# Kernel optimization log

Hardware: AMD Instinct MI355X
Metric: run time of the kernel (lower is better)

## Reference

```python
import jax, jax.numpy as jnp
import numpy as np
from math import lgamma

B = 8
RES = 64
RES_OUT = 32
L_IN = RES // 2 - 1        # 31
L_OUT = RES_OUT // 2 - 1   # 15
SPINS_IN = (0, 1)
SPINS_OUT = (0, 1, 2)
C_IN = 64
C_OUT = 128
K_IN = (L_IN + 1) ** 2     # 1024 coefficients, ordered by (ell, m): idx = ell^2 + (m + ell)
K_OUT = (L_OUT + 1) ** 2   # 256
EPS_BN = 1e-5
EPS_NL = 1e-6


def _wigner_d_col(l, s, thetas):
    """Wigner small-d column d^l_{m,-s}(theta) for m in [-l, l]; (2l+1, n_theta)."""
    n = -s
    out = np.zeros((2 * l + 1, thetas.size))
    if l < abs(s):
        return out
    cb = np.cos(thetas / 2.0)
    sb = np.sin(thetas / 2.0)
    for mi, m in enumerate(range(-l, l + 1)):
        pref = 0.5 * (lgamma(l + m + 1) + lgamma(l - m + 1)
                      + lgamma(l + n + 1) + lgamma(l - n + 1))
        acc = np.zeros_like(thetas)
        for k in range(max(0, n - m), min(l + n, l - m) + 1):
            lg = pref - (lgamma(l + n - k + 1) + lgamma(k + 1)
                         + lgamma(m - n + k + 1) + lgamma(l - m - k + 1))
            acc += ((-1.0) ** (m - n + k)) * np.exp(lg) \
                   * cb ** (2 * l + n - m - 2 * k) * sb ** (m - n + 2 * k)
        out[mi] = acc
    return out


def _sylm_grid(spin, ell_max, res):
    """Spin-weighted spherical harmonics sampled on equiangular grid: (K, res, res)."""
    thetas = (np.arange(res) + 0.5) * np.pi / res
    phis = np.arange(res) * 2.0 * np.pi / res
    Y = np.zeros(((ell_max + 1) ** 2, res, res), dtype=np.complex64)
    phase = np.exp(1j * np.outer(np.arange(-ell_max, ell_max + 1), phis))
    for l in range(ell_max + 1):
        d = _wigner_d_col(l, spin, thetas)               # (2l+1, res)
        norm = np.sqrt((2 * l + 1) / (4.0 * np.pi))
        for mi, m in enumerate(range(-l, l + 1)):
            Y[l * l + mi] = (((-1.0) ** m) * norm * d[mi][:, None]
                             * phase[m + ell_max][None, :])
    return Y


# Deterministic transform constants (computed once at import).
_THETA = (np.arange(RES) + 0.5) * np.pi / RES
_QUAD_W = (np.sin(_THETA) * (np.pi / RES) * (2.0 * np.pi / RES)).astype(np.float32)
Y_IN = np.stack([_sylm_grid(s, L_IN, RES) for s in SPINS_IN])          # (Si,K_IN,RES,RES)
Y_IN_W = (np.conj(Y_IN) * _QUAD_W[None, None, :, None]).astype(np.complex64)
Y_OUT = np.stack([_sylm_grid(s, L_OUT, RES_OUT) for s in SPINS_OUT])   # (So,K_OUT,32,32)
ELL_OUT = np.floor(np.sqrt(np.arange(K_OUT))).astype(np.int32)         # degree of each coeff


def setup_inputs() -> dict:
    key = jax.random.key(0)
    ks = jax.random.split(key, 8)
    shape_x = (B, RES, RES, len(SPINS_IN), C_IN)
    kern_shape = (L_IN + 1, len(SPINS_IN), len(SPINS_OUT), C_IN, C_OUT)
    scale = 1.0 / np.sqrt(len(SPINS_IN) * C_IN)
    return {
        "x_real": jax.random.normal(ks[0], shape_x, jnp.float32),
        "x_imag": jax.random.normal(ks[1], shape_x, jnp.float32),
        "kernel_real": jax.random.normal(ks[2], kern_shape, jnp.float32) * scale,
        "kernel_imag": jax.random.normal(ks[3], kern_shape, jnp.float32) * scale,
        "gamma": jax.random.uniform(ks[4], (len(SPINS_OUT), C_OUT), jnp.float32, 0.5, 1.5),
        "beta_real": jax.random.normal(ks[5], (len(SPINS_OUT), C_OUT), jnp.float32) * 0.1,
        "beta_imag": jax.random.normal(ks[6], (len(SPINS_OUT), C_OUT), jnp.float32) * 0.1,
        "nonlin_bias": jax.random.normal(ks[7], (len(SPINS_OUT), C_OUT), jnp.float32) * 0.1,
    }


def _forward(x_real, x_imag, kernel_real, kernel_imag, gamma,
             beta_real, beta_imag, nonlin_bias):
    x = x_real + 1j * x_imag                                   # (B,RES,RES,Si,Ci)
    # Forward spin-weighted spherical harmonic transform, per input spin.
    coeffs = jnp.einsum('btpiu,iktp->bkiu', x, jnp.asarray(Y_IN_W))  # (B,K_IN,Si,Ci)
    # Spectral pooling: keep degrees ell <= L_OUT (coeffs ordered by ell).
    coeffs = coeffs[:, :K_OUT]
    # Per-degree spectral convolution mixing spins and channels.
    kernel = (kernel_real + 1j * kernel_imag)[jnp.asarray(ELL_OUT)]  # (K_OUT,Si,So,Ci,Co)
    out_coeffs = jnp.einsum('bkiu,kisud->bksd', coeffs, kernel)      # (B,K_OUT,So,Co)
    # Inverse transform on the downsampled grid, per output spin.
    fmap = jnp.einsum('bksd,sktp->btpsd', out_coeffs, jnp.asarray(Y_OUT))
    # Equivariant batch norm: mean subtraction only for spin 0 channels.
    spin0 = (jnp.asarray(np.array(SPINS_OUT)) == 0)[:, None]         # (So,1)
    mean = jnp.mean(fmap, axis=(0, 1, 2)) * spin0                    # (So,Co)
    centered = fmap - mean
    var = jnp.mean(jnp.abs(centered) ** 2, axis=(0, 1, 2))           # (So,Co)
    beta = (beta_real + 1j * beta_imag) * spin0
    y = centered * (gamma / jnp.sqrt(var + EPS_BN)) + beta
    # Magnitude nonlinearity: y * relu(|y| + b) / (|y| + eps).
    mag = jnp.abs(y)
    return y * (jax.nn.relu(mag + nonlin_bias) / (mag + EPS_NL))


def reference(x_real, x_imag, kernel_real, kernel_imag, gamma,
              beta_real, beta_imag, nonlin_bias):
    return _forward(x_real, x_imag, kernel_real, kernel_imag, gamma,
                    beta_real, beta_imag, nonlin_bias)
```

## Files before the change

### kernel.cpp

```cpp
#include <hip/hip_runtime.h>
#include <hip/hip_fp16.h>
#include <math.h>


#define PI_D 3.14159265358979323846

#define OFF_A_IN    ((size_t)24320)
#define OFF_A_OUT   ((size_t)155648)
#define OFF_STATS   ((size_t)254208)
#define OFF_R1      ((size_t)260608)
#define OFF_R2      ((size_t)25426688)
#define OFF_W       ((size_t)67108864)

typedef float f4ev __attribute__((ext_vector_type(4)));

__device__ __forceinline__ void nts_h2(__half2* p, __half2 v) {
    union { __half2 h; unsigned u; } c;
    c.h = v;
    __builtin_nontemporal_store(c.u, (unsigned*)p);
}
__device__ __forceinline__ __half2 ntl_h2(const __half2* p) {
    union { unsigned u; __half2 h; } c;
    c.u = __builtin_nontemporal_load((unsigned*)p);
    return c.h;
}
__device__ __forceinline__ void nts_f4(float4* p, float a, float b, float c,
                                       float d) {
    f4ev t;
    t.x = a; t.y = b; t.z = c; t.w = d;
    __builtin_nontemporal_store(t, (f4ev*)p);
}
__device__ __forceinline__ void nts_f(float* p, float v) {
    __builtin_nontemporal_store(v, p);
}

__constant__ double LF[31] = {
    0.0, 0.0, 0.6931471805599453, 1.791759469228055, 3.1780538303479458,
    4.787491742782046, 6.579251212010101, 8.525161361065415,
    10.604602902745251, 12.801827480081469, 15.104412573075516,
    17.502307845873887, 19.987214495661885, 22.552163853123425,
    25.19122118273868, 27.89927138384089, 30.671860106080672,
    33.50507345013689, 36.39544520803305, 39.339884187199495,
    42.335616460753485, 45.38013889847691, 48.47118135183523,
    51.60667556776438, 54.78472939811232, 58.00360522298052,
    61.261701761002, 64.55753862700634, 67.88974313718154,
    71.25703896716801, 74.65823634883016};

__device__ inline int isqrt_k(int k) {
    int l = (int)sqrtf((float)k + 0.5f);
    while (l * l > k) --l;
    while ((l + 1) * (l + 1) <= k) ++l;
    return l;
}

__device__ double wigner_d_rec(int l, int m, int n, double theta) {
    int an = n < 0 ? -n : n;
    int am = m < 0 ? -m : m;
    if (l < an || l < am) return 0.0;
    int kmin = max(0, n - m), kmax = min(l + n, l - m);
    if (kmax < kmin) return 0.0;
    double cb = cos(0.5 * theta), sb = sin(0.5 * theta);
    double pref = 0.5 * (LF[l + m] + LF[l - m] + LF[l + n] + LF[l - n]);
    double lterm = pref
        - (LF[l + n - kmin] + LF[kmin] + LF[m - n + kmin] + LF[l - m - kmin])
        + (double)(2 * l + n - m - 2 * kmin) * log(cb)
        + (double)(m - n + 2 * kmin) * log(sb);
    double term = exp(lterm);
    if ((m - n + kmin) & 1) term = -term;
    double r = (sb * sb) / (cb * cb);
    double acc = term;
    for (int k = kmin; k < kmax; ++k) {
        term *= -((double)((l + n - k) * (l - m - k)) * r)
                / ((double)((k + 1) * (m - n + k + 1)));
        acc += term;
    }
    return acc;
}

__global__ __launch_bounds__(512, 2) void k_phi_tables(const float* __restrict__ xr,
                                                       const float* __restrict__ xi,
                                                       __half2* __restrict__ F,
                                                       float* __restrict__ A_in,
                                                       float* __restrict__ A_out,
                                                       float* __restrict__ stats,
                                                       const float* __restrict__ kr,
                                                       const float* __restrict__ ki,
                                                       float4* __restrict__ W) {
    if (blockIdx.x >= 512) {
        if (blockIdx.x >= 627) {
            int e0 = (blockIdx.x - 627) * 512 + threadIdx.x;
            const float2* kr2 = (const float2*)kr;
            const float2* ki2 = (const float2*)ki;
#pragma unroll
            for (int j = 0; j < 16; ++j) {
                int e = e0 + j * 24576;
                int dp = e & 63, r = e >> 6;
                float2 a = kr2[(size_t)r * 64 + dp];
                float2 b = ki2[(size_t)r * 64 + dp];
                nts_f4(&W[e], a.x, a.y, b.x, b.y);
            }
            return;
        }
        int idx = (blockIdx.x - 512) * 512 + threadIdx.x;
        if (idx < 32768) {
            int t = idx & 63, k = (idx >> 6) & 255, i = idx >> 14;
            int l = isqrt_k(k);
            int m = k - l * l - l;
            double theta = ((double)t + 0.5) * PI_D / 64.0;
            double w = sin(theta) * (PI_D / 64.0) * (2.0 * PI_D / 64.0);
            double norm = sqrt((2.0 * l + 1.0) / (4.0 * PI_D));
            double d = wigner_d_rec(l, m, -i, theta);
            A_in[idx] = (float)(((m & 1) ? -1.0 : 1.0) * norm * w * d);
            return;
        }
        idx -= 32768;
        if (idx < 24576) {
            int t = idx & 31, k = (idx >> 5) & 255, s = idx >> 13;
            int l = isqrt_k(k);
            int m = k - l * l - l;
            double theta = ((double)t + 0.5) * PI_D / 32.0;
            double norm = sqrt((2.0 * l + 1.0) / (4.0 * PI_D));
            double d = wigner_d_rec(l, m, -s, theta);
            A_out[idx] = (float)(((m & 1) ? -1.0 : 1.0) * norm * d);
            return;
        }
        idx -= 24576;
        if (idx < 1152) stats[idx] = 0.f;
        return;
    }
    int bt = blockIdx.x;
    int iu = threadIdx.x & 127, mh = threadIdx.x >> 7;
    int mi0 = mh * 8;
    float2 acc[8], w[8], st[8];
#pragma unroll
    for (int j = 0; j < 8; ++j) {
        int m = mi0 + j - 15;
        float sy, sx;
        __sincosf(-(float)m * (float)(PI_D / 32.0), &sy, &sx);
        st[j] = make_float2(sx, sy);
        w[j] = make_float2(1.f, 0.f);
        acc[j] = make_float2(0.f, 0.f);
    }
    const float* xrb = xr + (size_t)bt * 8192 + iu;
    const float* xib = xi + (size_t)bt * 8192 + iu;
    for (int p = 0; p < 32; ++p) {
        float a  = xrb[(size_t)p * 128];
        float b  = xib[(size_t)p * 128];
        float a2 = xrb[(size_t)(p + 32) * 128];
        float b2 = xib[(size_t)(p + 32) * 128];
        float sar = a + a2, sai = b + b2;
        float dar = a - a2, dai = b - b2;
#pragma unroll
        for (int j = 0; j < 8; ++j) {
            float ur = (j & 1) ? sar : dar;
            float ui = (j & 1) ? sai : dai;
            acc[j].x += ur * w[j].x - ui * w[j].y;
            acc[j].y += ur * w[j].y + ui * w[j].x;
            float nx = w[j].x * st[j].x - w[j].y * st[j].y;
            w[j].y = w[j].x * st[j].y + w[j].y * st[j].x;
            w[j].x = nx;
        }
    }
    __half2* Fb = F + (size_t)bt * 31 * 128 + iu;
#pragma unroll
    for (int j = 0; j < 8; ++j) {
        int mi = mi0 + j;
        if (mi < 31) nts_h2(&Fb[(size_t)mi * 128], __float22half2_rn(acc[j]));
    }
}

__global__ __launch_bounds__(256, 4) void k_theta_in(const __half2* __restrict__ F,
                                                     const float* __restrict__ A_in,
                                                     __half2* __restrict__ coeffs) {
    __shared__ float A[16][64];
    __shared__ float2 red[2][16][64];
    int mi = blockIdx.x, b = blockIdx.y, z = blockIdx.z;
    int m = mi - 15;
    int am = m < 0 ? -m : m;
    int tid = threadIdx.x;
    for (int idx = tid; idx < 1024; idx += 256) {
        int j = idx >> 6, t = idx & 63;
        float v = 0.f;
        if (j >= am) v = A_in[((size_t)z * 256 + (j * j + j + m)) * 64 + t];
        A[j][t] = v;
    }
    __syncthreads();
    int iu_l = tid & 63, th = tid >> 6;
    int iu = z * 64 + iu_l;
    float2 acc[16];
#pragma unroll
    for (int j = 0; j < 16; ++j) acc[j] = make_float2(0.f, 0.f);
    const __half2* Fb = F + ((size_t)b * 64 * 31 + mi) * 128 + iu;
    for (int tt = 0; tt < 16; ++tt) {
        int t = th * 16 + tt;
        float2 f = __half22float2(ntl_h2(&Fb[(size_t)t * 31 * 128]));
#pragma unroll
        for (int j = 0; j < 16; ++j) {
            float a = A[j][t];
            acc[j].x += a * f.x;
            acc[j].y += a * f.y;
        }
    }
    if (th >= 2) {
#pragma unroll
        for (int j = 0; j < 16; ++j) red[th - 2][j][iu_l] = acc[j];
    }
    __syncthreads();
    if (th < 2) {
#pragma unroll
        for (int j = 0; j < 16; ++j) {
            float2 r = red[th][j][iu_l];
            acc[j].x += r.x;
            acc[j].y += r.y;
        }
    }
    __syncthreads();
    if (th == 1) {
#pragma unroll
        for (int j = 0; j < 16; ++j) red[0][j][iu_l] = acc[j];
    }
    __syncthreads();
    if (th == 0) {
#pragma unroll
        for (int j = 0; j < 16; ++j) {
            if (j >= am) {
                float2 r = red[0][j][iu_l];
                nts_h2(&coeffs[((size_t)b * 256 + (j * j + j + m)) * 128 + iu],
                       __float22half2_rn(
                           make_float2(acc[j].x + r.x, acc[j].y + r.y)));
            }
        }
    }
}

__global__ __launch_bounds__(384) void k_mix(const __half2* __restrict__ coeffs,
                                             const float4* __restrict__ W,
                                             __half2* __restrict__ oc) {
    __shared__ float2 cs[4][128];
    __shared__ float2 red[192][4][2];
    int bx = blockIdx.x;
    int k = ((bx & 7) << 5) + (bx >> 3);
    int b0 = blockIdx.y * 4;
    int tid = threadIdx.x;
    for (int idx = tid; idx < 512; idx += 384) {
        int bb = idx >> 7, iuu = idx & 127;
        cs[bb][iuu] = __half22float2(
            ntl_h2(&coeffs[((size_t)(b0 + bb) * 256 + k) * 128 + iuu]));
    }
    __syncthreads();
    int ih = tid >= 192 ? 1 : 0;
    int r = tid - ih * 192;
    int s = r >> 6, dp = r & 63;
    int l = isqrt_k(k);
    float2 acc[4][2];
#pragma unroll
    for (int bb = 0; bb < 4; ++bb) {
        acc[bb][0] = make_float2(0.f, 0.f);
        acc[bb][1] = make_float2(0.f, 0.f);
    }
    const float4* Wb = W + (size_t)(6 * l + 3 * ih + s) * 4096 + dp;
    float4 cur[4];
#pragma unroll
    for (int j = 0; j < 4; ++j) cur[j] = Wb[(size_t)j * 64];
    for (int g = 0; g < 16; ++g) {
        float4 nxt[4];
        if (g < 15) {
#pragma unroll
            for (int j = 0; j < 4; ++j)
                nxt[j] = Wb[(size_t)((g + 1) * 4 + j) * 64];
        }
#pragma unroll
        for (int j = 0; j < 4; ++j) {
            int iu = ih * 64 + g * 4 + j;
            float2 wr = make_float2(cur[j].x, cur[j].y);
            float2 wi = make_float2(cur[j].z, cur[j].w);
#pragma unroll
            for (int bb = 0; bb < 4; ++bb) {
                float2 cv = cs[bb][iu];
                acc[bb][0].x += cv.x * wr.x - cv.y * wi.x;
                acc[bb][0].y += cv.x * wi.x + cv.y * wr.x;
                acc[bb][1].x += cv.x * wr.y - cv.y * wi.y;
                acc[bb][1].y += cv.x * wi.y + cv.y * wr.y;
            }
        }
        if (g < 15) {
#pragma unroll
            for (int j = 0; j < 4; ++j) cur[j] = nxt[j];
        }
    }
    if (ih == 1) {
#pragma unroll
        for (int bb = 0; bb < 4; ++bb) {
            red[r][bb][0] = acc[bb][0];
            red[r][bb][1] = acc[bb][1];
        }
    }
    __syncthreads();
    if (ih == 0) {
#pragma unroll
        for (int bb = 0; bb < 4; ++bb) {
            float2 r0 = red[r][bb][0];
            float2 r1 = red[r][bb][1];
            size_t o = ((size_t)(b0 + bb) * 256 + k) * 384 + s * 128 + 2 * dp;
            nts_h2(&oc[o], __float22half2_rn(
                make_float2(acc[bb][0].x + r0.x, acc[bb][0].y + r0.y)));
            nts_h2(&oc[o + 1], __float22half2_rn(
                make_float2(acc[bb][1].x + r1.x, acc[bb][1].y + r1.y)));
        }
    }
}

__global__ __launch_bounds__(192, 4) void k_theta_out(const __half2* __restrict__ oc,
                                                      const float* __restrict__ A_out,
                                                      __half2* __restrict__ G,
                                                      float* __restrict__ ssr,
                                                      float* __restrict__ ssi,
                                                      float* __restrict__ ssq) {
    __shared__ float Ao[3][16][32];
    int mi = blockIdx.x, b = blockIdx.y, z = blockIdx.z;
    int m = mi - 15;
    int am = m < 0 ? -m : m;
    int tid = threadIdx.x;
    for (int idx = tid; idx < 1536; idx += 192) {
        int s = idx >> 9, j = (idx >> 5) & 15, t = idx & 31;
        float v = 0.f;
        if (j >= am) v = A_out[((size_t)s * 256 + (j * j + j + m)) * 32 + t];
        Ao[s][j][t] = v;
    }
    __syncthreads();
    int sd = z * 192 + tid;
    int s = sd >> 7;
    float2 c[16];
#pragma unroll
    for (int j = 0; j < 16; ++j) {
        c[j] = make_float2(0.f, 0.f);
        if (j >= am)
            c[j] = __half22float2(
                ntl_h2(&oc[((size_t)b * 256 + (j * j + j + m)) * 384 + sd]));
    }
    float sq = 0.f, sr = 0.f, si = 0.f;
    for (int t = 0; t < 32; ++t) {
        float fr = 0.f, fi = 0.f;
#pragma unroll
        for (int j = 0; j < 16; ++j) {
            float a = Ao[s][j][t];
            fr += a * c[j].x;
            fi += a * c[j].y;
        }
        nts_h2(&G[(((size_t)b * 32 + t) * 31 + mi) * 384 + sd],
               __float22half2_rn(make_float2(fr, fi)));
        sq += fr * fr + fi * fi;
        if (mi == 15) { sr += fr; si += fi; }
    }
    atomicAdd(&ssq[sd], sq);
    if (mi == 15) {
        atomicAdd(&ssr[sd], sr);
        atomicAdd(&ssi[sd], si);
    }
}

__global__ __launch_bounds__(192, 2) void k_synth_final(const __half2* __restrict__ G,
                                                        const float* __restrict__ ssr,
                                                        const float* __restrict__ ssi,
                                                        const float* __restrict__ ssq,
                                                        const float* __restrict__ gamma,
                                                        const float* __restrict__ betar,
                                                        const float* __restrict__ betai,
                                                        const float* __restrict__ bias,
                                                        float* __restrict__ out) {
    int bt = blockIdx.x;
    int sd = blockIdx.y * 192 + threadIdx.x;
    int s = sd >> 7;
    float2 g[31], st[31];
#pragma unroll
    for (int mi = 0; mi < 31; ++mi) {
        g[mi] = __half22float2(ntl_h2(&G[((size_t)bt * 31 + mi) * 384 + sd]));
        float sy, sx;
        __sincosf((float)(mi - 15) * (float)(PI_D / 16.0), &sy, &sx);
        st[mi] = make_float2(sx, sy);
    }
    const float invN = 1.0f / 256.0f;
    float mur = 0.f, mui = 0.f;
    if (s == 0) { mur = ssr[sd] * invN; mui = ssi[sd] * invN; }
    float var = ssq[sd] * invN - (mur * mur + mui * mui);
    float scale = gamma[sd] / sqrtf(var + 1e-5f);
    float br = (s == 0) ? betar[sd] : 0.f;
    float bi = (s == 0) ? betai[sd] : 0.f;
    float bb = bias[sd];
    float* ob = out + (size_t)bt * 32 * 384 + sd;
    for (int p = 0; p < 16; ++p) {
        float fr = 0.f, fi = 0.f, fr2 = 0.f, fi2 = 0.f;
#pragma unroll
        for (int mi = 0; mi < 31; ++mi) {
            fr += g[mi].x;
            fi += g[mi].y;
            if (mi & 1) { fr2 += g[mi].x; fi2 += g[mi].y; }
            else        { fr2 -= g[mi].x; fi2 -= g[mi].y; }
        }
        {
            float yr = (fr - mur) * scale + br;
            float yi = (fi - mui) * scale + bi;
            float mag = sqrtf(yr * yr + yi * yi);
            float f = fmaxf(mag + bb, 0.f) / (mag + 1e-6f);
            nts_f(&ob[(size_t)p * 384], yr * f);
        }
        {
            float yr = (fr2 - mur) * scale + br;
            float yi = (fi2 - mui) * scale + bi;
            float mag = sqrtf(yr * yr + yi * yi);
            float f = fmaxf(mag + bb, 0.f) / (mag + 1e-6f);
            nts_f(&ob[(size_t)(p + 16) * 384], yr * f);
        }
#pragma unroll
        for (int mi = 0; mi < 31; ++mi) {
            float nx = g[mi].x * st[mi].x - g[mi].y * st[mi].y;
            g[mi].y = g[mi].x * st[mi].y + g[mi].y * st[mi].x;
            g[mi].x = nx;
        }
    }
}

extern "C" void kernel_launch(void* const* d_in, const int* in_sizes, int n_in,
                              void* d_out, int out_size, void* d_ws, size_t ws_size,
                              hipStream_t stream) {
    const float* xr    = (const float*)d_in[0];
    const float* xi    = (const float*)d_in[1];
    const float* kr    = (const float*)d_in[2];
    const float* ki    = (const float*)d_in[3];
    const float* gamma = (const float*)d_in[4];
    const float* betar = (const float*)d_in[5];
    const float* betai = (const float*)d_in[6];
    const float* bias  = (const float*)d_in[7];
    float* out = (float*)d_out;

    char* ws = (char*)d_ws;
    float*   A_in   = (float*)(ws + OFF_A_IN);
    float*   A_out  = (float*)(ws + OFF_A_OUT);
    float*   stats  = (float*)(ws + OFF_STATS);
    float*   ssr    = stats;
    float*   ssi    = stats + 384;
    float*   ssq    = stats + 768;
    __half2* F      = (__half2*)(ws + OFF_R1);
    __half2* oc     = (__half2*)(ws + OFF_R1);
    __half2* coeffs = (__half2*)(ws + OFF_R2);
    __half2* G      = (__half2*)(ws + OFF_R2);
    float4*  W      = (float4*)(ws + OFF_W);

    k_phi_tables<<<675, 512, 0, stream>>>(xr, xi, F, A_in, A_out, stats, kr, ki, W);
    k_theta_in<<<dim3(31, 8, 2), 256, 0, stream>>>(F, A_in, coeffs);
    k_mix<<<dim3(256, 2), 384, 0, stream>>>(coeffs, W, oc);
    k_theta_out<<<dim3(31, 8, 2), 192, 0, stream>>>(oc, A_out, G, ssr, ssi, ssq);
    k_synth_final<<<dim3(256, 2), 192, 0, stream>>>(G, ssr, ssi, ssq,
                                                    gamma, betar, betai, bias, out);
}
```

Before: 177.7 us.

## Fuse theta-in Legendre transform with channel mixing into one kernel

Merges k_theta_in and k_mix into one kernel. Each block handles one degree l, one batch and one quarter of output channels, computing that l's coefficients in shared memory chunk by chunk over m and mixing them immediately. This drops the coeffs round-trip through global memory and one launch, and oc moves to its own buffer. In exchange each block redoes the theta reduction for its l (four times across dq), uses a serial 64-step loop per thread, and load is uneven across l.

```diff
diff --git a/kernel.cpp b/kernel.cpp
--- a/kernel.cpp
+++ b/kernel.cpp
@@ -10,6 +10,7 @@
 #define OFF_STATS   ((size_t)254208)
 #define OFF_R1      ((size_t)260608)
 #define OFF_R2      ((size_t)25426688)
+#define OFF_OC      ((size_t)41943040)
 #define OFF_W       ((size_t)67108864)
 
 typedef float f4ev __attribute__((ext_vector_type(4)));
@@ -169,144 +170,95 @@
     }
 }
 
-__global__ __launch_bounds__(256, 4) void k_theta_in(const __half2* __restrict__ F,
-                                                     const float* __restrict__ A_in,
-                                                     __half2* __restrict__ coeffs) {
-    __shared__ float A[16][64];
-    __shared__ float2 red[2][16][64];
-    int mi = blockIdx.x, b = blockIdx.y, z = blockIdx.z;
-    int m = mi - 15;
-    int am = m < 0 ? -m : m;
-    int tid = threadIdx.x;
-    for (int idx = tid; idx < 1024; idx += 256) {
-        int j = idx >> 6, t = idx & 63;
-        float v = 0.f;
-        if (j >= am) v = A_in[((size_t)z * 256 + (j * j + j + m)) * 64 + t];
-        A[j][t] = v;
-    }
-    __syncthreads();
-    int iu_l = tid & 63, th = tid >> 6;
-    int iu = z * 64 + iu_l;
-    float2 acc[16];
-#pragma unroll
-    for (int j = 0; j < 16; ++j) acc[j] = make_float2(0.f, 0.f);
-    const __half2* Fb = F + ((size_t)b * 64 * 31 + mi) * 128 + iu;
-    for (int tt = 0; tt < 16; ++tt) {
-        int t = th * 16 + tt;
-        float2 f = __half22float2(ntl_h2(&Fb[(size_t)t * 31 * 128]));
-#pragma unroll
-        for (int j = 0; j < 16; ++j) {
-            float a = A[j][t];
-            acc[j].x += a * f.x;
-            acc[j].y += a * f.y;
-        }
-    }
-    if (th >= 2) {
-#pragma unroll
-        for (int j = 0; j < 16; ++j) red[th - 2][j][iu_l] = acc[j];
-    }
-    __syncthreads();
-    if (th < 2) {
-#pragma unroll
-        for (int j = 0; j < 16; ++j) {
-            float2 r = red[th][j][iu_l];
-            acc[j].x += r.x;
-            acc[j].y += r.y;
-        }
-    }
-    __syncthreads();
-    if (th == 1) {
-#pragma unroll
-        for (int j = 0; j < 16; ++j) red[0][j][iu_l] = acc[j];
-    }
-    __syncthreads();
-    if (th == 0) {
-#pragma unroll
-        for (int j = 0; j < 16; ++j) {
-            if (j >= am) {
-                float2 r = red[0][j][iu_l];
-                nts_h2(&coeffs[((size_t)b * 256 + (j * j + j + m)) * 128 + iu],
-                       __float22half2_rn(
-                           make_float2(acc[j].x + r.x, acc[j].y + r.y)));
+__global__ __launch_bounds__(512) void k_theta_mix(const __half2* __restrict__ F,
+                                                   const float* __restrict__ A_in,
+                                                   const float4* __restrict__ W,
+                                                   __half2* __restrict__ oc) {
+    __shared__ float As[4][2][64];
+    __shared__ float2 cl[4][128];
+    __shared__ float2 red[192][2];
+    int bid = blockIdx.x, tid = threadIdx.x;
+    int l = 15 - (bid >> 5);
+    int r = bid & 31;
+    int b = r >> 2, dq = r & 3;
+    int nm = 2 * l + 1;
+    int nchunk = (nm + 3) >> 2;
+
+    int mmA = tid >> 7, iuA = tid & 127;
+    int iA = iuA >> 6;
+    int mmB = tid / 96;
+    int rB = tid % 96;
+    int sB = rB / 32;
+    int r2 = rB % 32;
+    int dplB = r2 >> 1, ihB = r2 & 1;
+    int dp = dq * 16 + dplB;
+    int redi = (mmB * 3 + sB) * 16 + dplB;
+
+    for (int c = 0; c < nchunk; ++c) {
+        {
+            int mm = tid >> 7, rest = tid & 127;
+            int i = rest >> 6, t = rest & 63;
+            int moff = 4 * c + mm;
+            float v = 0.f;
+            if (moff < nm) {
+                int k = l * l + moff;
+                v = A_in[((size_t)i * 256 + k) * 64 + t];
             }
-        }
-    }
-}
-
-__global__ __launch_bounds__(384) void k_mix(const __half2* __restrict__ coeffs,
-                                             const float4* __restrict__ W,
-                                             __half2* __restrict__ oc) {
-    __shared__ float2 cs[4][128];
-    __shared__ float2 red[192][4][2];
-    int bx = blockIdx.x;
-    int k = ((bx & 7) << 5) + (bx >> 3);
-    int b0 = blockIdx.y * 4;
-    int tid = threadIdx.x;
-    for (int idx = tid; idx < 512; idx += 384) {
-        int bb = idx >> 7, iuu = idx & 127;
-        cs[bb][iuu] = __half22float2(
-            ntl_h2(&coeffs[((size_t)(b0 + bb) * 256 + k) * 128 + iuu]));
-    }
-    __syncthreads();
-    int ih = tid >= 192 ? 1 : 0;
-    int r = tid - ih * 192;
-    int s = r >> 6, dp = r & 63;
-    int l = isqrt_k(k);
-    float2 acc[4][2];
-#pragma unroll
-    for (int bb = 0; bb < 4; ++bb) {
-        acc[bb][0] = make_float2(0.f, 0.f);
-        acc[bb][1] = make_float2(0.f, 0.f);
-    }
-    const float4* Wb = W + (size_t)(6 * l + 3 * ih + s) * 4096 + dp;
-    float4 cur[4];
-#pragma unroll
-    for (int j = 0; j < 4; ++j) cur[j] = Wb[(size_t)j * 64];
-    for (int g = 0; g < 16; ++g) {
-        float4 nxt[4];
-        if (g < 15) {
-#pragma unroll
-            for (int j = 0; j < 4; ++j)
-                nxt[j] = Wb[(size_t)((g + 1) * 4 + j) * 64];
-        }
-#pragma unroll
-        for (int j = 0; j < 4; ++j) {
-            int iu = ih * 64 + g * 4 + j;
-            float2 wr = make_float2(cur[j].x, cur[j].y);
-            float2 wi = make_float2(cur[j].z, cur[j].w);
-#pragma unroll
-            for (int bb = 0; bb < 4; ++bb) {
-                float2 cv = cs[bb][iu];
-                acc[bb][0].x += cv.x * wr.x - cv.y * wi.x;
-                acc[bb][0].y += cv.x * wi.x + cv.y * wr.x;
-                acc[bb][1].x += cv.x * wr.y - cv.y * wi.y;
-                acc[bb][1].y += cv.x * wi.y + cv.y * wr.y;
+            As[mm][i][t] = v;
+        }
+        __syncthreads();
+        {
+            int moff = 4 * c + mmA;
+            float ax = 0.f, ay = 0.f;
+            if (moff < nm) {
+                int mi = moff + 15 - l;
+                const __half2* Fb =
+                    F + ((size_t)b * 64 * 31 + mi) * 128 + iuA;
+                const float* Ai = As[mmA][iA];
+#pragma unroll 8
+                for (int t = 0; t < 64; ++t) {
+                    float2 f = __half22float2(ntl_h2(&Fb[(size_t)t * 31 * 128]));
+                    float a = Ai[t];
+                    ax += a * f.x;
+                    ay += a * f.y;
+                }
             }
-        }
-        if (g < 15) {
-#pragma unroll
-            for (int j = 0; j < 4; ++j) cur[j] = nxt[j];
-        }
-    }
-    if (ih == 1) {
-#pragma unroll
-        for (int bb = 0; bb < 4; ++bb) {
-            red[r][bb][0] = acc[bb][0];
-            red[r][bb][1] = acc[bb][1];
-        }
-    }
-    __syncthreads();
-    if (ih == 0) {
-#pragma unroll
-        for (int bb = 0; bb < 4; ++bb) {
-            float2 r0 = red[r][bb][0];
-            float2 r1 = red[r][bb][1];
-            size_t o = ((size_t)(b0 + bb) * 256 + k) * 384 + s * 128 + 2 * dp;
+            cl[mmA][iuA] = make_float2(ax, ay);
+        }
+        __syncthreads();
+        int moffB = 4 * c + mmB;
+        bool on = (tid < 384) && (moffB < nm);
+        float2 a0 = make_float2(0.f, 0.f);
+        float2 a1 = make_float2(0.f, 0.f);
+        if (on) {
+            const float4* Wb =
+                W + (size_t)(6 * l + 3 * ihB + sB) * 4096 + dp;
+            const float2* cm = cl[mmB] + ihB * 64;
+            for (int u = 0; u < 64; ++u) {
+                float4 wv = Wb[(size_t)u * 64];
+                float2 cv = cm[u];
+                a0.x += cv.x * wv.x - cv.y * wv.z;
+                a0.y += cv.x * wv.z + cv.y * wv.x;
+                a1.x += cv.x * wv.y - cv.y * wv.w;
+                a1.y += cv.x * wv.w + cv.y * wv.y;
+            }
+            if (ihB == 1) {
+                red[redi][0] = a0;
+                red[redi][1] = a1;
+            }
+        }
+        __syncthreads();
+        if (on && ihB == 0) {
+            float2 r0 = red[redi][0];
+            float2 r1 = red[redi][1];
+            int k = l * l + moffB;
+            size_t o = ((size_t)b * 256 + k) * 384 + sB * 128 + 2 * dp;
             nts_h2(&oc[o], __float22half2_rn(
-                make_float2(acc[bb][0].x + r0.x, acc[bb][0].y + r0.y)));
+                make_float2(a0.x + r0.x, a0.y + r0.y)));
             nts_h2(&oc[o + 1], __float22half2_rn(
-                make_float2(acc[bb][1].x + r1.x, acc[bb][1].y + r1.y)));
-        }
+                make_float2(a1.x + r1.x, a1.y + r1.y)));
+        }
+        __syncthreads();
     }
 }
 
@@ -441,14 +393,12 @@
     float*   ssi    = stats + 384;
     float*   ssq    = stats + 768;
     __half2* F      = (__half2*)(ws + OFF_R1);
-    __half2* oc     = (__half2*)(ws + OFF_R1);
-    __half2* coeffs = (__half2*)(ws + OFF_R2);
     __half2* G      = (__half2*)(ws + OFF_R2);
+    __half2* oc     = (__half2*)(ws + OFF_OC);
     float4*  W      = (float4*)(ws + OFF_W);
 
     k_phi_tables<<<675, 512, 0, stream>>>(xr, xi, F, A_in, A_out, stats, kr, ki, W);
-    k_theta_in<<<dim3(31, 8, 2), 256, 0, stream>>>(F, A_in, coeffs);
-    k_mix<<<dim3(256, 2), 384, 0, stream>>>(coeffs, W, oc);
+    k_theta_mix<<<512, 512, 0, stream>>>(F, A_in, W, oc);
     k_theta_out<<<dim3(31, 8, 2), 192, 0, stream>>>(oc, A_out, G, ssr, ssi, ssq);
     k_synth_final<<<dim3(256, 2), 192, 0, stream>>>(G, ssr, ssi, ssq,
                                                     gamma, betar, betai, bias, out);
```

Result: slower. 251.3 us (+41.4%).
